# Optimization experiments

Hardware: AMD Instinct MI355X
Metric: run time of the kernel (lower is better)

Reference implementation:

```python
import jax, jax.numpy as jnp
import numpy as np

N_NODES = 50000
N_EDGES = 800000
NFEAT = 128
NHID = 128
NCLASS = 10
NUM_GRAPHS = 512


def setup_inputs() -> dict:
    key = jax.random.key(0)
    ks = jax.random.split(key, 12)
    x = jax.random.normal(ks[0], (N_NODES, NFEAT), dtype=jnp.float32)
    edge_index = jax.random.randint(ks[1], (2, N_EDGES), 0, N_NODES, dtype=jnp.int64)
    batch = jnp.sort(jax.random.randint(ks[2], (N_NODES,), 0, NUM_GRAPHS, dtype=jnp.int64))
    def glorot(k, fan_in, fan_out):
        lim = np.sqrt(6.0 / (fan_in + fan_out))
        return jax.random.uniform(k, (fan_in, fan_out), jnp.float32, -lim, lim)
    return {
        "x": x, "edge_index": edge_index, "batch": batch,
        "W0": glorot(ks[3], NFEAT, NHID), "b0": jnp.zeros((NHID,), jnp.float32),
        "W1": glorot(ks[4], NHID, NHID), "b1": jnp.zeros((NHID,), jnp.float32),
        "W2": glorot(ks[5], NHID, NHID), "b2": jnp.zeros((NHID,), jnp.float32),
        "lin_w": glorot(ks[6], NHID, NCLASS), "lin_b": jnp.zeros((NCLASS,), jnp.float32),
    }


def _gcn_norm(edge_index, n):
    # PyG GCNConv: add self-loops, symmetric normalization D^-1/2 A D^-1/2
    loop = jnp.arange(n, dtype=edge_index.dtype)
    src = jnp.concatenate([edge_index[0], loop])  # [E+N]
    dst = jnp.concatenate([edge_index[1], loop])
    deg = jax.ops.segment_sum(jnp.ones_like(dst, dtype=jnp.float32), dst, num_segments=n)
    dis = jnp.where(deg > 0, jax.lax.rsqrt(jnp.maximum(deg, 1.0)), 0.0)
    norm = dis[src] * dis[dst]  # [E+N]
    return src, dst, norm


def _gcn_conv(x, W, b, src, dst, norm, n):
    h = x @ W                              # [N, nhid]
    msg = h[src] * norm[:, None]           # gather + scale, [E+N, nhid]
    out = jax.ops.segment_sum(msg, dst, num_segments=n)
    return out + b


def reference(x, edge_index, batch, W0, b0, W1, b1, W2, b2, lin_w, lin_b):
    n = x.shape[0]
    src, dst, norm = _gcn_norm(edge_index, n)
    h = x
    for (W, b) in ((W0, b0), (W1, b1), (W2, b2)):
        h = jax.nn.relu(_gcn_conv(h, W, b, src, dst, norm, n))
    # global mean pool over graphs
    sums = jax.ops.segment_sum(h, batch, num_segments=NUM_GRAPHS)
    cnts = jax.ops.segment_sum(jnp.ones((n,), jnp.float32), batch, num_segments=NUM_GRAPHS)
    pooled = sums / jnp.maximum(cnts, 1.0)[:, None]  # [G, nhid]
    logits = pooled @ lin_w + lin_b
    return jax.nn.log_softmax(logits, axis=-1)
```

## Files before the change

### kernel.cpp

```cpp
#include <hip/hip_runtime.h>
#include <hip/hip_fp16.h>


#define FEAT 128
#define NCLASS 10
#define NB_MAX 512

typedef _Float16 h8 __attribute__((ext_vector_type(8)));
typedef float f4 __attribute__((ext_vector_type(4)));

__device__ inline int swz(int row, int cbyte) { return row * 256 + (cbyte ^ ((row & 7) << 4)); }

__device__ inline void gather_pad4(const h8* __restrict__ Hs, const int* __restrict__ csr,
                                   int s, int e, int lig, float* a0, float* a1) {
  int ep = s + ((e - s + 7) & ~7);
  for (int k = s; k < ep; k += 4) {
    int4 c = *(const int4*)&csr[k];
    h8 v0 = Hs[(size_t)c.x * 16 + lig];
    h8 v1 = Hs[(size_t)c.y * 16 + lig];
    h8 v2 = Hs[(size_t)c.z * 16 + lig];
    h8 v3 = Hs[(size_t)c.w * 16 + lig];
#pragma unroll
    for (int j = 0; j < 8; ++j) a0[j] += (float)v0[j];
#pragma unroll
    for (int j = 0; j < 8; ++j) a1[j] += (float)v1[j];
#pragma unroll
    for (int j = 0; j < 8; ++j) a0[j] += (float)v2[j];
#pragma unroll
    for (int j = 0; j < 8; ++j) a1[j] += (float)v3[j];
  }
}

__global__ void __launch_bounds__(256) prep_kernel(const int* __restrict__ ei,
                                                   int* __restrict__ bhist,
                                                   int ne, int nb, int epb, int hb,
                                                   const float* __restrict__ W0,
                                                   const float* __restrict__ W1,
                                                   const float* __restrict__ W2,
                                                   _Float16* __restrict__ Wt, int wtb,
                                                   const int* __restrict__ batch,
                                                   int* __restrict__ gstart, int n, int g) {
  int t = threadIdx.x;
  if (blockIdx.x >= hb + wtb) {
    int i = (blockIdx.x - hb - wtb) * 256 + t;
    if (i >= n) return;
    int bi = batch[i];
    int bp = (i == 0) ? -1 : batch[i - 1];
    for (int q = bp + 1; q <= bi; ++q) gstart[q] = i;
    if (i == n - 1)
      for (int q = bi + 1; q <= g; ++q) gstart[q] = n;
    return;
  }
  if (blockIdx.x >= hb) {
    int i = (blockIdx.x - hb) * 256 + t;
    if (i < 3 * FEAT * FEAT) {
      int l = i / (FEAT * FEAT);
      int r = i - l * (FEAT * FEAT);
      int nn = r >> 7, kk = r & 127;
      const float* W = (l == 0) ? W0 : (l == 1) ? W1 : W2;
      Wt[i] = (_Float16)W[kk * FEAT + nn];
    }
    return;
  }
  __shared__ int lh[NB_MAX];
  for (int i = t; i < nb; i += 256) lh[i] = 0;
  __syncthreads();
  int r0 = blockIdx.x * epb;
  int r1 = min(r0 + epb, ne);
  for (int k = r0 + t; k < r1; k += 256) atomicAdd(&lh[ei[ne + k] >> 7], 1);
  __syncthreads();
  for (int i = t; i < nb; i += 256)
    if (lh[i]) atomicAdd(&bhist[i], lh[i]);
}

__global__ void __launch_bounds__(512) bscan_kernel(const int* __restrict__ bhist,
                                                    int* __restrict__ bstart,
                                                    int* __restrict__ bcur,
                                                    int nb, int ne) {
  __shared__ int sh[512];
  int t = threadIdx.x;
  int v = (t < nb) ? bhist[t] : 0;
  sh[t] = v;
  __syncthreads();
  int x = v;
  for (int d = 1; d < 512; d <<= 1) {
    int y = (t >= d) ? sh[t - d] : 0;
    __syncthreads();
    x += y;
    sh[t] = x;
    __syncthreads();
  }
  if (t < nb) {
    bstart[t] = x - v;
    bcur[t] = x - v;
  }
  if (t == 0) bstart[nb] = ne;
}

__global__ void __launch_bounds__(256) scatter_kernel(const int* __restrict__ ei,
                                                      int* __restrict__ bcur,
                                                      unsigned* __restrict__ buf,
                                                      int ne, int nb, int epb) {
  __shared__ int lh[NB_MAX], lbs[NB_MAX];
  int t = threadIdx.x;
  for (int i = t; i < nb; i += 256) lh[i] = 0;
  __syncthreads();
  int r0 = blockIdx.x * epb;
  int r1 = min(r0 + epb, ne);
  for (int k = r0 + t; k < r1; k += 256) atomicAdd(&lh[ei[ne + k] >> 7], 1);
  __syncthreads();
  for (int i = t; i < nb; i += 256) {
    int c = lh[i];
    lbs[i] = c ? atomicAdd(&bcur[i], c) : 0;
    lh[i] = 0;
  }
  __syncthreads();
  for (int k = r0 + t; k < r1; k += 256) {
    int src = ei[k];
    int dst = ei[ne + k];
    int b = dst >> 7;
    int p = lbs[b] + atomicAdd(&lh[b], 1);
    buf[p] = (unsigned)src | ((unsigned)(dst & 127) << 25);
  }
}

__global__ void __launch_bounds__(256) bucket_build_kernel(const unsigned* __restrict__ buf,
                                                           const int* __restrict__ bstart,
                                                           int2* __restrict__ offend,
                                                           int* __restrict__ csr,
                                                           float* __restrict__ dis, int n) {
  __shared__ int cnt[128], cur[128], sh[128], ps[128];
  int b = blockIdx.x, t = threadIdx.x;
  int e0 = bstart[b], e1 = bstart[b + 1];
  int pb = ((e0 + 7) & ~7) + 1024 * b;
  if (t < 128) cnt[t] = 0;
  __syncthreads();
  for (int k = e0 + t; k < e1; k += 256) atomicAdd(&cnt[buf[k] >> 25], 1);
  __syncthreads();
  int v = 0, pdv = 0;
  if (t < 128) {
    v = cnt[t];
    pdv = (v + 7) & ~7;
    sh[t] = pdv;
  }
  __syncthreads();
  int x = pdv;
  for (int d = 1; d < 128; d <<= 1) {
    int y = (t < 128 && t >= d) ? sh[t - d] : 0;
    __syncthreads();
    if (t < 128) {
      x += y;
      sh[t] = x;
    }
    __syncthreads();
  }
  if (t < 128) {
    int node = (b << 7) + t;
    int st = x - pdv;
    ps[t] = st;
    cur[t] = st;
    if (node < n) {
      offend[node] = make_int2(pb + st, pb + st + v);
      dis[node] = rsqrtf((float)(v + 1));
    }
  }
  __syncthreads();
  for (int k = e0 + t; k < e1; k += 256) {
    unsigned u = buf[k];
    int d = u >> 25;
    int p = atomicAdd(&cur[d], 1);
    csr[pb + p] = (int)(u & 0x1FFFFFFu);
  }
  __syncthreads();
  if (t < 128) {
    int pd = (cnt[t] + 7) & ~7;
    for (int q = cnt[t]; q < pd; ++q) csr[pb + ps[t] + q] = n;
  }
}

__global__ void __launch_bounds__(256) gemm_mfma_kernel(const float* __restrict__ Xf,
                                                        const _Float16* __restrict__ Wt,
                                                        const float* __restrict__ dis,
                                                        _Float16* __restrict__ Hs, int n) {
  __shared__ _Float16 st[64 * FEAT];
  int tid = threadIdx.x;
  int w = tid >> 6, lane = tid & 63;
  int l15 = lane & 15, hi = lane >> 4;

  int rowA = blockIdx.x * 64 + w * 16 + l15;
  int rA = min(rowA, n - 1);

  f4 acc[8];
#pragma unroll
  for (int nb = 0; nb < 8; ++nb) acc[nb] = (f4)(0.f);

#pragma unroll
  for (int kk = 0; kk < FEAT; kk += 32) {
    int ko = kk + hi * 8;
    h8 a;
    float4 x0 = *(const float4*)&Xf[(size_t)rA * FEAT + ko];
    float4 x1 = *(const float4*)&Xf[(size_t)rA * FEAT + ko + 4];
    a[0] = (_Float16)x0.x; a[1] = (_Float16)x0.y; a[2] = (_Float16)x0.z; a[3] = (_Float16)x0.w;
    a[4] = (_Float16)x1.x; a[5] = (_Float16)x1.y; a[6] = (_Float16)x1.z; a[7] = (_Float16)x1.w;
#pragma unroll
    for (int nb = 0; nb < 8; ++nb) {
      h8 bfr = *(const h8*)&Wt[(nb * 16 + l15) * FEAT + ko];
      acc[nb] = __builtin_amdgcn_mfma_f32_16x16x32_f16(a, bfr, acc[nb], 0, 0, 0);
    }
  }

  float dv[4];
#pragma unroll
  for (int r = 0; r < 4; ++r) {
    int grow = blockIdx.x * 64 + w * 16 + hi * 4 + r;
    dv[r] = dis[min(grow, n - 1)];
  }
#pragma unroll
  for (int nb = 0; nb < 8; ++nb)
#pragma unroll
    for (int r = 0; r < 4; ++r)
      st[(w * 16 + hi * 4 + r) * FEAT + nb * 16 + l15] = (_Float16)(acc[nb][r] * dv[r]);
  __syncthreads();

  int rowbase = blockIdx.x * 64;
#pragma unroll
  for (int i = tid; i < 64 * FEAT / 8; i += 256) {
    int row = rowbase + (i >> 4);
    if (row < n)
      *(uint4*)&Hs[(size_t)row * FEAT + (i & 15) * 8] =
          *(const uint4*)&st[(i >> 4) * FEAT + (i & 15) * 8];
  }
}

__global__ void __launch_bounds__(512, 6) fused_kernel(const h8* __restrict__ Hs_in,
                                                       const int* __restrict__ csr,
                                                       const int2* __restrict__ offend,
                                                       const float* __restrict__ dis,
                                                       const float* __restrict__ bias,
                                                       const _Float16* __restrict__ Wt,
                                                       _Float16* __restrict__ Hs_out, int n) {
  __shared__ char xsb[64 * 256];
  int tid = threadIdx.x;
  int w = tid >> 6, lane = tid & 63;
  int grp = lane >> 4, lig = lane & 15;
  int row0 = blockIdx.x * 64;
  int g32 = w * 4 + grp;

  float4 b0 = ((const float4*)bias)[lig * 2];
  float4 b1 = ((const float4*)bias)[lig * 2 + 1];
  float bb[8] = {b0.x, b0.y, b0.z, b0.w, b1.x, b1.y, b1.z, b1.w};

#pragma unroll
  for (int m = 0; m < 2; ++m) {
    int ar = g32 * 2 + m;
    int nd = min(row0 + ar, n - 1);
    int2 oe = offend[nd];
    float a0[8], a1[8];
    h8 v = Hs_in[(size_t)nd * 16 + lig];
#pragma unroll
    for (int j = 0; j < 8; ++j) {
      a0[j] = (float)v[j];
      a1[j] = 0.f;
    }
    gather_pad4(Hs_in, csr, oe.x, oe.y, lig, a0, a1);
    float d = dis[nd];
    h8 o;
#pragma unroll
    for (int j = 0; j < 8; ++j)
      o[j] = (_Float16)fmaxf(fmaf(d, a0[j] + a1[j], bb[j]), 0.f);
    *(h8*)(xsb + swz(ar, lig * 16)) = o;
  }
  __syncthreads();

  int l15 = lane & 15, hi = lane >> 4;
  int strip = w & 3, ch = w >> 2;
  f4 acc[4];
#pragma unroll
  for (int nb = 0; nb < 4; ++nb) acc[nb] = (f4)(0.f);
#pragma unroll
  for (int kk = 0; kk < FEAT; kk += 32) {
    int ko = kk + hi * 8;
    h8 a = *(const h8*)(xsb + swz(strip * 16 + l15, ko * 2));
#pragma unroll
    for (int nb = 0; nb < 4; ++nb) {
      h8 bfr = *(const h8*)&Wt[(ch * 64 + nb * 16 + l15) * FEAT + ko];
      acc[nb] = __builtin_amdgcn_mfma_f32_16x16x32_f16(a, bfr, acc[nb], 0, 0, 0);
    }
  }

  float dv[4];
#pragma unroll
  for (int r = 0; r < 4; ++r) {
    int grow = row0 + strip * 16 + hi * 4 + r;
    dv[r] = dis[min(grow, n - 1)];
  }
  __syncthreads();
#pragma unroll
  for (int nb = 0; nb < 4; ++nb)
#pragma unroll
    for (int r = 0; r < 4; ++r) {
      int srow = strip * 16 + hi * 4 + r;
      *(_Float16*)(xsb + swz(srow, (ch * 64 + nb * 16 + l15) * 2)) =
          (_Float16)(acc[nb][r] * dv[r]);
    }
  __syncthreads();
#pragma unroll
  for (int i = tid; i < 64 * FEAT / 8; i += 512) {
    int row = row0 + (i >> 4);
    if (row < n)
      *(uint4*)&Hs_out[(size_t)row * FEAT + (i & 15) * 8] =
          *(const uint4*)(xsb + swz(i >> 4, (i & 15) * 16));
  }
}

__global__ void __launch_bounds__(512, 6) agg_kernel(const h8* __restrict__ Hs,
                                                     const int* __restrict__ csr,
                                                     const int2* __restrict__ offend,
                                                     const float* __restrict__ dis,
                                                     const float* __restrict__ bias,
                                                     h8* __restrict__ out, int n) {
  int tid = threadIdx.x;
  int g32 = tid >> 4, lig = tid & 15;
  int row0 = blockIdx.x * 64;

  float4 b0 = ((const float4*)bias)[lig * 2];
  float4 b1 = ((const float4*)bias)[lig * 2 + 1];
  float bb[8] = {b0.x, b0.y, b0.z, b0.w, b1.x, b1.y, b1.z, b1.w};

#pragma unroll
  for (int m = 0; m < 2; ++m) {
    int node = row0 + g32 * 2 + m;
    if (node < n) {
      int2 oe = offend[node];
      float a0[8], a1[8];
      h8 v = Hs[(size_t)node * 16 + lig];
#pragma unroll
      for (int j = 0; j < 8; ++j) {
        a0[j] = (float)v[j];
        a1[j] = 0.f;
      }
      gather_pad4(Hs, csr, oe.x, oe.y, lig, a0, a1);
      float d = dis[node];
      h8 o;
#pragma unroll
      for (int j = 0; j < 8; ++j)
        o[j] = (_Float16)fmaxf(fmaf(d, a0[j] + a1[j], bb[j]), 0.f);
      out[(size_t)node * 16 + lig] = o;
    }
  }
}

__global__ void __launch_bounds__(128) pool_kernel(const __half* __restrict__ h,
                                                   const int* __restrict__ gstart,
                                                   const float* __restrict__ lw,
                                                   const float* __restrict__ lb,
                                                   float* __restrict__ out) {
  int g = blockIdx.x;
  int t = threadIdx.x;
  int s = gstart[g];
  int e = gstart[g + 1];
  float a0 = 0.f, a1 = 0.f, a2 = 0.f, a3 = 0.f;
  int i = s;
  for (; i + 4 <= e; i += 4) {
    a0 += __half2float(h[(size_t)i * FEAT + t]);
    a1 += __half2float(h[(size_t)(i + 1) * FEAT + t]);
    a2 += __half2float(h[(size_t)(i + 2) * FEAT + t]);
    a3 += __half2float(h[(size_t)(i + 3) * FEAT + t]);
  }
  for (; i < e; ++i) a0 += __half2float(h[(size_t)i * FEAT + t]);
  float acc = a0 + a1 + a2 + a3;
  float cnt = (float)(e - s);
  float pooled = acc / fmaxf(cnt, 1.f);
  __shared__ float lds[FEAT];
  __shared__ float logits[NCLASS];
  lds[t] = pooled;
  __syncthreads();
  if (t < NCLASS) {
    float z = lb[t];
    for (int k = 0; k < FEAT; ++k) z += lds[k] * lw[k * NCLASS + t];
    logits[t] = z;
  }
  __syncthreads();
  if (t < NCLASS) {
    float m = logits[0];
#pragma unroll
    for (int c = 1; c < NCLASS; ++c) m = fmaxf(m, logits[c]);
    float ssum = 0.f;
#pragma unroll
    for (int c = 0; c < NCLASS; ++c) ssum += expf(logits[c] - m);
    out[(size_t)g * NCLASS + t] = logits[t] - m - logf(ssum);
  }
}

extern "C" void kernel_launch(void* const* d_in, const int* in_sizes, int n_in,
                              void* d_out, int out_size, void* d_ws, size_t ws_size,
                              hipStream_t stream) {
  const float* x = (const float*)d_in[0];
  const int* ei = (const int*)d_in[1];
  const int* batch = (const int*)d_in[2];
  const float* W0 = (const float*)d_in[3];
  const float* b0 = (const float*)d_in[4];
  const float* W1 = (const float*)d_in[5];
  const float* b1 = (const float*)d_in[6];
  const float* W2 = (const float*)d_in[7];
  const float* b2 = (const float*)d_in[8];
  const float* lw = (const float*)d_in[9];
  const float* lb = (const float*)d_in[10];

  int n = in_sizes[2];
  int ne = in_sizes[1] / 2;
  int g = out_size / NCLASS;
  int nb = (n + 127) >> 7;
  int hblocks = 120;
  int epb = (ne + hblocks - 1) / hblocks;
  int wtblocks = (3 * FEAT * FEAT + 255) / 256;
  int bndblocks = (n + 255) / 256;

  char* ws = (char*)d_ws;
  size_t p = 0;
  auto alloc = [&](size_t bytes) {
    size_t cur = p;
    p += (bytes + 255) & ~(size_t)255;
    return cur;
  };
  int2* offend = (int2*)(ws + alloc((size_t)n * 8));
  int* csr = (int*)(ws + alloc(((size_t)ne + 1024 * nb + 64) * 4));
  int* bhist = (int*)(ws + alloc((size_t)NB_MAX * 4));
  int* bstart = (int*)(ws + alloc((size_t)(NB_MAX + 1) * 4));
  int* bcur = (int*)(ws + alloc((size_t)NB_MAX * 4));
  int* gstart = (int*)(ws + alloc((size_t)(g + 1) * 4));
  float* dis = (float*)(ws + alloc((size_t)n * 4));
  unsigned* buf = (unsigned*)(ws + alloc((size_t)ne * 4));
  _Float16* Wt = (_Float16*)(ws + alloc((size_t)3 * FEAT * FEAT * 2));
  _Float16* HA = (_Float16*)(ws + alloc((size_t)(n + 1) * FEAT * 2));
  _Float16* HB = (_Float16*)(ws + alloc((size_t)(n + 1) * FEAT * 2));

  hipMemsetAsync(bhist, 0, NB_MAX * 4, stream);
  hipMemsetAsync(HA + (size_t)n * FEAT, 0, FEAT * 2, stream);
  hipMemsetAsync(HB + (size_t)n * FEAT, 0, FEAT * 2, stream);

  prep_kernel<<<hblocks + wtblocks + bndblocks, 256, 0, stream>>>(
      ei, bhist, ne, nb, epb, hblocks, W0, W1, W2, Wt, wtblocks, batch, gstart, n, g);
  bscan_kernel<<<1, 512, 0, stream>>>(bhist, bstart, bcur, nb, ne);
  scatter_kernel<<<hblocks, 256, 0, stream>>>(ei, bcur, buf, ne, nb, epb);
  bucket_build_kernel<<<nb, 256, 0, stream>>>(buf, bstart, offend, csr, dis, n);

  int gblocks = (n + 63) / 64;
  gemm_mfma_kernel<<<gblocks, 256, 0, stream>>>(x, Wt, dis, HA, n);
  fused_kernel<<<gblocks, 512, 0, stream>>>((const h8*)HA, csr, offend, dis, b0,
                                            Wt + (size_t)1 * FEAT * FEAT, HB, n);
  fused_kernel<<<gblocks, 512, 0, stream>>>((const h8*)HB, csr, offend, dis, b1,
                                            Wt + (size_t)2 * FEAT * FEAT, HA, n);
  agg_kernel<<<gblocks, 512, 0, stream>>>((const h8*)HA, csr, offend, dis, b2, (h8*)HB, n);

  pool_kernel<<<g, 128, 0, stream>>>((const __half*)HB, gstart, lw, lb, (float*)d_out);
}
```

Baseline: 221.9 us.

## Split hidden features into four column-quarter planes for cache-local gathers

Stores the fp16 hidden matrices as four separate planes of 32 features each, so each gather pass touches only a 3.2MB quarter table that fits better in L2. The aggregation loops now iterate over the quarters and load 4 bytes per lane instead of 16. CSR padding drops from multiples of 8 to multiples of 4, and the memset of the padding row moves into the prep kernel. The cost is four passes over the CSR indices and narrower per-lane loads, which issue more memory instructions per edge.

Result: slower. 238.2 us (+7.3%).

```diff
diff --git a/kernel.cpp b/kernel.cpp
--- a/kernel.cpp
+++ b/kernel.cpp
@@ -11,24 +11,9 @@
 
 __device__ inline int swz(int row, int cbyte) { return row * 256 + (cbyte ^ ((row & 7) << 4)); }
 
-__device__ inline void gather_pad4(const h8* __restrict__ Hs, const int* __restrict__ csr,
-                                   int s, int e, int lig, float* a0, float* a1) {
-  int ep = s + ((e - s + 7) & ~7);
-  for (int k = s; k < ep; k += 4) {
-    int4 c = *(const int4*)&csr[k];
-    h8 v0 = Hs[(size_t)c.x * 16 + lig];
-    h8 v1 = Hs[(size_t)c.y * 16 + lig];
-    h8 v2 = Hs[(size_t)c.z * 16 + lig];
-    h8 v3 = Hs[(size_t)c.w * 16 + lig];
-#pragma unroll
-    for (int j = 0; j < 8; ++j) a0[j] += (float)v0[j];
-#pragma unroll
-    for (int j = 0; j < 8; ++j) a1[j] += (float)v1[j];
-#pragma unroll
-    for (int j = 0; j < 8; ++j) a0[j] += (float)v2[j];
-#pragma unroll
-    for (int j = 0; j < 8; ++j) a1[j] += (float)v3[j];
-  }
+__device__ inline float2 uh2f2(unsigned u) {
+  __half2 h = *reinterpret_cast<__half2*>(&u);
+  return make_float2(__low2float(h), __high2float(h));
 }
 
 __global__ void __launch_bounds__(256) prep_kernel(const int* __restrict__ ei,
@@ -39,8 +24,18 @@
                                                    const float* __restrict__ W2,
                                                    _Float16* __restrict__ Wt, int wtb,
                                                    const int* __restrict__ batch,
-                                                   int* __restrict__ gstart, int n, int g) {
+                                                   int* __restrict__ gstart, int n, int g,
+                                                   unsigned* __restrict__ HQA32,
+                                                   unsigned* __restrict__ HQB32, int nblk) {
   int t = threadIdx.x;
+  if (blockIdx.x == nblk - 1) {
+    if (t < 128) {
+      unsigned* H = (t >> 6) ? HQB32 : HQA32;
+      int q = (t >> 4) & 3;
+      H[(size_t)q * (n + 1) * 16 + (size_t)n * 16 + (t & 15)] = 0u;
+    }
+    return;
+  }
   if (blockIdx.x >= hb + wtb) {
     int i = (blockIdx.x - hb - wtb) * 256 + t;
     if (i >= n) return;
@@ -140,7 +135,7 @@
   int v = 0, pdv = 0;
   if (t < 128) {
     v = cnt[t];
-    pdv = (v + 7) & ~7;
+    pdv = (v + 3) & ~3;
     sh[t] = pdv;
   }
   __syncthreads();
@@ -173,7 +168,7 @@
   }
   __syncthreads();
   if (t < 128) {
-    int pd = (cnt[t] + 7) & ~7;
+    int pd = (cnt[t] + 3) & ~3;
     for (int q = cnt[t]; q < pd; ++q) csr[pb + ps[t] + q] = n;
   }
 }
@@ -181,7 +176,7 @@
 __global__ void __launch_bounds__(256) gemm_mfma_kernel(const float* __restrict__ Xf,
                                                         const _Float16* __restrict__ Wt,
                                                         const float* __restrict__ dis,
-                                                        _Float16* __restrict__ Hs, int n) {
+                                                        uint4* __restrict__ H4, int n) {
   __shared__ _Float16 st[64 * FEAT];
   int tid = threadIdx.x;
   int w = tid >> 6, lane = tid & 63;
@@ -223,22 +218,23 @@
   __syncthreads();
 
   int rowbase = blockIdx.x * 64;
-#pragma unroll
-  for (int i = tid; i < 64 * FEAT / 8; i += 256) {
+  int qs4 = (n + 1) * 4;
+#pragma unroll
+  for (int i = tid; i < 64 * 16; i += 256) {
     int row = rowbase + (i >> 4);
+    int c = i & 15, q = c >> 2;
     if (row < n)
-      *(uint4*)&Hs[(size_t)row * FEAT + (i & 15) * 8] =
-          *(const uint4*)&st[(i >> 4) * FEAT + (i & 15) * 8];
-  }
-}
-
-__global__ void __launch_bounds__(512, 6) fused_kernel(const h8* __restrict__ Hs_in,
+      H4[(size_t)q * qs4 + row * 4 + (c & 3)] = *(const uint4*)&st[(i >> 4) * FEAT + c * 8];
+  }
+}
+
+__global__ void __launch_bounds__(512, 6) fused_kernel(const unsigned* __restrict__ HQin,
                                                        const int* __restrict__ csr,
                                                        const int2* __restrict__ offend,
                                                        const float* __restrict__ dis,
                                                        const float* __restrict__ bias,
                                                        const _Float16* __restrict__ Wt,
-                                                       _Float16* __restrict__ Hs_out, int n) {
+                                                       uint4* __restrict__ H4out, int n) {
   __shared__ char xsb[64 * 256];
   int tid = threadIdx.x;
   int w = tid >> 6, lane = tid & 63;
@@ -246,29 +242,45 @@
   int row0 = blockIdx.x * 64;
   int g32 = w * 4 + grp;
 
-  float4 b0 = ((const float4*)bias)[lig * 2];
-  float4 b1 = ((const float4*)bias)[lig * 2 + 1];
-  float bb[8] = {b0.x, b0.y, b0.z, b0.w, b1.x, b1.y, b1.z, b1.w};
-
+  int nds[2];
+  int2 oes[2];
+  float ds[2];
 #pragma unroll
   for (int m = 0; m < 2; ++m) {
-    int ar = g32 * 2 + m;
-    int nd = min(row0 + ar, n - 1);
-    int2 oe = offend[nd];
-    float a0[8], a1[8];
-    h8 v = Hs_in[(size_t)nd * 16 + lig];
-#pragma unroll
-    for (int j = 0; j < 8; ++j) {
-      a0[j] = (float)v[j];
-      a1[j] = 0.f;
-    }
-    gather_pad4(Hs_in, csr, oe.x, oe.y, lig, a0, a1);
-    float d = dis[nd];
-    h8 o;
-#pragma unroll
-    for (int j = 0; j < 8; ++j)
-      o[j] = (_Float16)fmaxf(fmaf(d, a0[j] + a1[j], bb[j]), 0.f);
-    *(h8*)(xsb + swz(ar, lig * 16)) = o;
+    nds[m] = min(row0 + g32 * 2 + m, n - 1);
+    oes[m] = offend[nds[m]];
+    ds[m] = dis[nds[m]];
+  }
+  int qstep = (n + 1) * 16;
+
+  for (int q = 0; q < 4; ++q) {
+    const unsigned* T = HQin + (size_t)q * qstep;
+    float2 bq = ((const float2*)bias)[q * 16 + lig];
+#pragma unroll
+    for (int m = 0; m < 2; ++m) {
+      int nd = nds[m];
+      float2 sv = uh2f2(T[(size_t)nd * 16 + lig]);
+      float ax = sv.x, ay = sv.y, bx = 0.f, by = 0.f;
+      int s = oes[m].x;
+      int ep = s + ((oes[m].y - s + 3) & ~3);
+      for (int k = s; k < ep; k += 4) {
+        int4 c = *(const int4*)&csr[k];
+        unsigned u0 = T[(size_t)c.x * 16 + lig];
+        unsigned u1 = T[(size_t)c.y * 16 + lig];
+        unsigned u2 = T[(size_t)c.z * 16 + lig];
+        unsigned u3 = T[(size_t)c.w * 16 + lig];
+        float2 v0 = uh2f2(u0), v1 = uh2f2(u1), v2 = uh2f2(u2), v3 = uh2f2(u3);
+        ax += v0.x; ay += v0.y;
+        bx += v1.x; by += v1.y;
+        ax += v2.x; ay += v2.y;
+        bx += v3.x; by += v3.y;
+      }
+      float ox = fmaxf(fmaf(ds[m], ax + bx, bq.x), 0.f);
+      float oy = fmaxf(fmaf(ds[m], ay + by, bq.y), 0.f);
+      __half2 hv = __floats2half2_rn(ox, oy);
+      int ar = g32 * 2 + m;
+      *(unsigned*)(xsb + swz(ar, q * 64 + lig * 4)) = *(unsigned*)&hv;
+    }
   }
   __syncthreads();
 
@@ -304,48 +316,67 @@
           (_Float16)(acc[nb][r] * dv[r]);
     }
   __syncthreads();
-#pragma unroll
-  for (int i = tid; i < 64 * FEAT / 8; i += 512) {
+  int qs4 = (n + 1) * 4;
+#pragma unroll
+  for (int i = tid; i < 64 * 16; i += 512) {
     int row = row0 + (i >> 4);
+    int c = i & 15, q = c >> 2;
     if (row < n)
-      *(uint4*)&Hs_out[(size_t)row * FEAT + (i & 15) * 8] =
-          *(const uint4*)(xsb + swz(i >> 4, (i & 15) * 16));
-  }
-}
-
-__global__ void __launch_bounds__(512, 6) agg_kernel(const h8* __restrict__ Hs,
+      H4out[(size_t)q * qs4 + row * 4 + (c & 3)] =
+          *(const uint4*)(xsb + swz(i >> 4, c * 16));
+  }
+}
+
+__global__ void __launch_bounds__(512, 6) agg_kernel(const unsigned* __restrict__ HQin,
                                                      const int* __restrict__ csr,
                                                      const int2* __restrict__ offend,
                                                      const float* __restrict__ dis,
                                                      const float* __restrict__ bias,
-                                                     h8* __restrict__ out, int n) {
+                                                     unsigned* __restrict__ out32, int n) {
   int tid = threadIdx.x;
   int g32 = tid >> 4, lig = tid & 15;
   int row0 = blockIdx.x * 64;
 
-  float4 b0 = ((const float4*)bias)[lig * 2];
-  float4 b1 = ((const float4*)bias)[lig * 2 + 1];
-  float bb[8] = {b0.x, b0.y, b0.z, b0.w, b1.x, b1.y, b1.z, b1.w};
-
+  int nds[2];
+  int2 oes[2];
+  float ds[2];
+  bool val[2];
 #pragma unroll
   for (int m = 0; m < 2; ++m) {
     int node = row0 + g32 * 2 + m;
-    if (node < n) {
-      int2 oe = offend[node];
-      float a0[8], a1[8];
-      h8 v = Hs[(size_t)node * 16 + lig];
-#pragma unroll
-      for (int j = 0; j < 8; ++j) {
-        a0[j] = (float)v[j];
-        a1[j] = 0.f;
+    val[m] = node < n;
+    nds[m] = min(node, n - 1);
+    oes[m] = offend[nds[m]];
+    ds[m] = dis[nds[m]];
+  }
+  int qstep = (n + 1) * 16;
+
+  for (int q = 0; q < 4; ++q) {
+    const unsigned* T = HQin + (size_t)q * qstep;
+    float2 bq = ((const float2*)bias)[q * 16 + lig];
+#pragma unroll
+    for (int m = 0; m < 2; ++m) {
+      int nd = nds[m];
+      float2 sv = uh2f2(T[(size_t)nd * 16 + lig]);
+      float ax = sv.x, ay = sv.y, bx = 0.f, by = 0.f;
+      int s = oes[m].x;
+      int ep = s + ((oes[m].y - s + 3) & ~3);
+      for (int k = s; k < ep; k += 4) {
+        int4 c = *(const int4*)&csr[k];
+        unsigned u0 = T[(size_t)c.x * 16 + lig];
+        unsigned u1 = T[(size_t)c.y * 16 + lig];
+        unsigned u2 = T[(size_t)c.z * 16 + lig];
+        unsigned u3 = T[(size_t)c.w * 16 + lig];
+        float2 v0 = uh2f2(u0), v1 = uh2f2(u1), v2 = uh2f2(u2), v3 = uh2f2(u3);
+        ax += v0.x; ay += v0.y;
+        bx += v1.x; by += v1.y;
+        ax += v2.x; ay += v2.y;
+        bx += v3.x; by += v3.y;
       }
-      gather_pad4(Hs, csr, oe.x, oe.y, lig, a0, a1);
-      float d = dis[node];
-      h8 o;
-#pragma unroll
-      for (int j = 0; j < 8; ++j)
-        o[j] = (_Float16)fmaxf(fmaf(d, a0[j] + a1[j], bb[j]), 0.f);
-      out[(size_t)node * 16 + lig] = o;
+      float ox = fmaxf(fmaf(ds[m], ax + bx, bq.x), 0.f);
+      float oy = fmaxf(fmaf(ds[m], ay + by, bq.y), 0.f);
+      __half2 hv = __floats2half2_rn(ox, oy);
+      if (val[m]) out32[(size_t)nds[m] * 64 + q * 16 + lig] = *(unsigned*)&hv;
     }
   }
 }
@@ -415,6 +446,7 @@
   int epb = (ne + hblocks - 1) / hblocks;
   int wtblocks = (3 * FEAT * FEAT + 255) / 256;
   int bndblocks = (n + 255) / 256;
+  int prep_total = hblocks + wtblocks + bndblocks + 1;
 
   char* ws = (char*)d_ws;
   size_t p = 0;
@@ -432,26 +464,26 @@
   float* dis = (float*)(ws + alloc((size_t)n * 4));
   unsigned* buf = (unsigned*)(ws + alloc((size_t)ne * 4));
   _Float16* Wt = (_Float16*)(ws + alloc((size_t)3 * FEAT * FEAT * 2));
-  _Float16* HA = (_Float16*)(ws + alloc((size_t)(n + 1) * FEAT * 2));
-  _Float16* HB = (_Float16*)(ws + alloc((size_t)(n + 1) * FEAT * 2));
+  unsigned* HQA = (unsigned*)(ws + alloc((size_t)(n + 1) * FEAT * 2));
+  unsigned* HQB = (unsigned*)(ws + alloc((size_t)(n + 1) * FEAT * 2));
+  unsigned* HR = (unsigned*)(ws + alloc((size_t)n * FEAT * 2));
 
   hipMemsetAsync(bhist, 0, NB_MAX * 4, stream);
-  hipMemsetAsync(HA + (size_t)n * FEAT, 0, FEAT * 2, stream);
-  hipMemsetAsync(HB + (size_t)n * FEAT, 0, FEAT * 2, stream);
-
-  prep_kernel<<<hblocks + wtblocks + bndblocks, 256, 0, stream>>>(
-      ei, bhist, ne, nb, epb, hblocks, W0, W1, W2, Wt, wtblocks, batch, gstart, n, g);
+
+  prep_kernel<<<prep_total, 256, 0, stream>>>(ei, bhist, ne, nb, epb, hblocks, W0, W1, W2,
+                                              Wt, wtblocks, batch, gstart, n, g, HQA, HQB,
+                                              prep_total);
   bscan_kernel<<<1, 512, 0, stream>>>(bhist, bstart, bcur, nb, ne);
   scatter_kernel<<<hblocks, 256, 0, stream>>>(ei, bcur, buf, ne, nb, epb);
   bucket_build_kernel<<<nb, 256, 0, stream>>>(buf, bstart, offend, csr, dis, n);
 
   int gblocks = (n + 63) / 64;
-  gemm_mfma_kernel<<<gblocks, 256, 0, stream>>>(x, Wt, dis, HA, n);
-  fused_kernel<<<gblocks, 512, 0, stream>>>((const h8*)HA, csr, offend, dis, b0,
-                                            Wt + (size_t)1 * FEAT * FEAT, HB, n);
-  fused_kernel<<<gblocks, 512, 0, stream>>>((const h8*)HB, csr, offend, dis, b1,
-                                            Wt + (size_t)2 * FEAT * FEAT, HA, n);
-  agg_kernel<<<gblocks, 512, 0, stream>>>((const h8*)HA, csr, offend, dis, b2, (h8*)HB, n);
-
-  pool_kernel<<<g, 128, 0, stream>>>((const __half*)HB, gstart, lw, lb, (float*)d_out);
-}
+  gemm_mfma_kernel<<<gblocks, 256, 0, stream>>>(x, Wt, dis, (uint4*)HQA, n);
+  fused_kernel<<<gblocks, 512, 0, stream>>>(HQA, csr, offend, dis, b0,
+                                            Wt + (size_t)1 * FEAT * FEAT, (uint4*)HQB, n);
+  fused_kernel<<<gblocks, 512, 0, stream>>>(HQB, csr, offend, dis, b1,
+                                            Wt + (size_t)2 * FEAT * FEAT, (uint4*)HQA, n);
+  agg_kernel<<<gblocks, 512, 0, stream>>>(HQA, csr, offend, dis, b2, HR, n);
+
+  pool_kernel<<<g, 128, 0, stream>>>((const __half*)HR, gstart, lw, lb, (float*)d_out);
+}
```

## Partition CSR neighbors by source-range chunks and sync blocks per chunk for L2 locality

Applied to the files above, without the earlier changes.

The CSR build now sorts each node's neighbors into four source-index ranges, each padded to a multiple of four, and stores per-chunk offsets. The gather loops in fused_kernel and agg_kernel walk the chunks in order with a __syncthreads between chunks. Workgroups then move through the feature table roughly in step, so the active working set of the random gathers is about a quarter of the table and should hit L2 or the MALL more often. The cost is more padding, extra metadata loads, block barriers that make each block wait for its slowest wave in every chunk, and a single accumulator chain per node instead of two.

Result: no change. 219.7 us (-1.0%).

```diff
diff --git a/kernel.cpp b/kernel.cpp
--- a/kernel.cpp
+++ b/kernel.cpp
@@ -10,26 +10,6 @@
 typedef float f4 __attribute__((ext_vector_type(4)));
 
 __device__ inline int swz(int row, int cbyte) { return row * 256 + (cbyte ^ ((row & 7) << 4)); }
-
-__device__ inline void gather_pad4(const h8* __restrict__ Hs, const int* __restrict__ csr,
-                                   int s, int e, int lig, float* a0, float* a1) {
-  int ep = s + ((e - s + 7) & ~7);
-  for (int k = s; k < ep; k += 4) {
-    int4 c = *(const int4*)&csr[k];
-    h8 v0 = Hs[(size_t)c.x * 16 + lig];
-    h8 v1 = Hs[(size_t)c.y * 16 + lig];
-    h8 v2 = Hs[(size_t)c.z * 16 + lig];
-    h8 v3 = Hs[(size_t)c.w * 16 + lig];
-#pragma unroll
-    for (int j = 0; j < 8; ++j) a0[j] += (float)v0[j];
-#pragma unroll
-    for (int j = 0; j < 8; ++j) a1[j] += (float)v1[j];
-#pragma unroll
-    for (int j = 0; j < 8; ++j) a0[j] += (float)v2[j];
-#pragma unroll
-    for (int j = 0; j < 8; ++j) a1[j] += (float)v3[j];
-  }
-}
 
 __global__ void __launch_bounds__(256) prep_kernel(const int* __restrict__ ei,
                                                    int* __restrict__ bhist,
@@ -126,25 +106,40 @@
 
 __global__ void __launch_bounds__(256) bucket_build_kernel(const unsigned* __restrict__ buf,
                                                            const int* __restrict__ bstart,
-                                                           int2* __restrict__ offend,
+                                                           int4* __restrict__ off4,
+                                                           int* __restrict__ oend,
                                                            int* __restrict__ csr,
-                                                           float* __restrict__ dis, int n) {
-  __shared__ int cnt[128], cur[128], sh[128], ps[128];
+                                                           float* __restrict__ dis,
+                                                           int n, int csize) {
+  __shared__ int cnt[512], cur[512], loc[512], sh[128];
   int b = blockIdx.x, t = threadIdx.x;
   int e0 = bstart[b], e1 = bstart[b + 1];
-  int pb = ((e0 + 7) & ~7) + 1024 * b;
-  if (t < 128) cnt[t] = 0;
-  __syncthreads();
-  for (int k = e0 + t; k < e1; k += 256) atomicAdd(&cnt[buf[k] >> 25], 1);
-  __syncthreads();
-  int v = 0, pdv = 0;
+  int pb = ((e0 + 7) & ~7) + 2048 * b;
+  for (int i = t; i < 512; i += 256) cnt[i] = 0;
+  __syncthreads();
+  for (int k = e0 + t; k < e1; k += 256) {
+    unsigned u = buf[k];
+    int src = (int)(u & 0x1FFFFFFu);
+    int d = u >> 25;
+    int c = (src >= 3 * csize) ? 3 : (src >= 2 * csize) ? 2 : (src >= csize) ? 1 : 0;
+    atomicAdd(&cnt[d * 4 + c], 1);
+  }
+  __syncthreads();
+  int tot = 0;
   if (t < 128) {
-    v = cnt[t];
-    pdv = (v + 7) & ~7;
-    sh[t] = pdv;
-  }
-  __syncthreads();
-  int x = pdv;
+    int p0 = (cnt[t * 4 + 0] + 3) & ~3;
+    int p1 = (cnt[t * 4 + 1] + 3) & ~3;
+    int p2 = (cnt[t * 4 + 2] + 3) & ~3;
+    int p3 = (cnt[t * 4 + 3] + 3) & ~3;
+    loc[t * 4 + 0] = 0;
+    loc[t * 4 + 1] = p0;
+    loc[t * 4 + 2] = p0 + p1;
+    loc[t * 4 + 3] = p0 + p1 + p2;
+    tot = p0 + p1 + p2 + p3;
+    sh[t] = tot;
+  }
+  __syncthreads();
+  int x = tot;
   for (int d = 1; d < 128; d <<= 1) {
     int y = (t < 128 && t >= d) ? sh[t - d] : 0;
     __syncthreads();
@@ -155,26 +150,39 @@
     __syncthreads();
   }
   if (t < 128) {
+    int st = pb + x - tot;
     int node = (b << 7) + t;
-    int st = x - pdv;
-    ps[t] = st;
-    cur[t] = st;
+    int s0 = st + loc[t * 4 + 0], s1 = st + loc[t * 4 + 1];
+    int s2 = st + loc[t * 4 + 2], s3 = st + loc[t * 4 + 3];
+    cur[t * 4 + 0] = s0;
+    cur[t * 4 + 1] = s1;
+    cur[t * 4 + 2] = s2;
+    cur[t * 4 + 3] = s3;
     if (node < n) {
-      offend[node] = make_int2(pb + st, pb + st + v);
+      off4[node] = make_int4(s0, s1, s2, s3);
+      oend[node] = st + tot;
+      int v = cnt[t * 4] + cnt[t * 4 + 1] + cnt[t * 4 + 2] + cnt[t * 4 + 3];
       dis[node] = rsqrtf((float)(v + 1));
     }
   }
   __syncthreads();
   for (int k = e0 + t; k < e1; k += 256) {
     unsigned u = buf[k];
+    int src = (int)(u & 0x1FFFFFFu);
     int d = u >> 25;
-    int p = atomicAdd(&cur[d], 1);
-    csr[pb + p] = (int)(u & 0x1FFFFFFu);
+    int c = (src >= 3 * csize) ? 3 : (src >= 2 * csize) ? 2 : (src >= csize) ? 1 : 0;
+    int p = atomicAdd(&cur[d * 4 + c], 1);
+    csr[p] = src;
   }
   __syncthreads();
   if (t < 128) {
-    int pd = (cnt[t] + 7) & ~7;
-    for (int q = cnt[t]; q < pd; ++q) csr[pb + ps[t] + q] = n;
+#pragma unroll
+    for (int c = 0; c < 4; ++c) {
+      int k0 = t * 4 + c;
+      int pad = ((cnt[k0] + 3) & ~3) - cnt[k0];
+      int base = cur[k0];
+      for (int q = 0; q < pad; ++q) csr[base + q] = n;
+    }
   }
 }
 
@@ -234,7 +242,8 @@
 
 __global__ void __launch_bounds__(512, 6) fused_kernel(const h8* __restrict__ Hs_in,
                                                        const int* __restrict__ csr,
-                                                       const int2* __restrict__ offend,
+                                                       const int4* __restrict__ off4,
+                                                       const int* __restrict__ oend,
                                                        const float* __restrict__ dis,
                                                        const float* __restrict__ bias,
                                                        const _Float16* __restrict__ Wt,
@@ -246,30 +255,61 @@
   int row0 = blockIdx.x * 64;
   int g32 = w * 4 + grp;
 
-  float4 b0 = ((const float4*)bias)[lig * 2];
-  float4 b1 = ((const float4*)bias)[lig * 2 + 1];
-  float bb[8] = {b0.x, b0.y, b0.z, b0.w, b1.x, b1.y, b1.z, b1.w};
-
-#pragma unroll
-  for (int m = 0; m < 2; ++m) {
-    int ar = g32 * 2 + m;
-    int nd = min(row0 + ar, n - 1);
-    int2 oe = offend[nd];
-    float a0[8], a1[8];
-    h8 v = Hs_in[(size_t)nd * 16 + lig];
-#pragma unroll
-    for (int j = 0; j < 8; ++j) {
-      a0[j] = (float)v[j];
-      a1[j] = 0.f;
-    }
-    gather_pad4(Hs_in, csr, oe.x, oe.y, lig, a0, a1);
-    float d = dis[nd];
-    h8 o;
-#pragma unroll
-    for (int j = 0; j < 8; ++j)
-      o[j] = (_Float16)fmaxf(fmaf(d, a0[j] + a1[j], bb[j]), 0.f);
-    *(h8*)(xsb + swz(ar, lig * 16)) = o;
-  }
+  int nd0 = min(row0 + g32 * 2, n - 1);
+  int nd1 = min(row0 + g32 * 2 + 1, n - 1);
+  int4 o0 = off4[nd0], o1 = off4[nd1];
+  int oe0 = oend[nd0], oe1 = oend[nd1];
+
+  float acc0[8], acc1[8];
+  h8 sv0 = Hs_in[(size_t)nd0 * 16 + lig];
+  h8 sv1 = Hs_in[(size_t)nd1 * 16 + lig];
+#pragma unroll
+  for (int j = 0; j < 8; ++j) {
+    acc0[j] = (float)sv0[j];
+    acc1[j] = (float)sv1[j];
+  }
+
+#pragma unroll
+  for (int c = 0; c < 4; ++c) {
+    int s0 = (c == 0) ? o0.x : (c == 1) ? o0.y : (c == 2) ? o0.z : o0.w;
+    int e0 = (c == 0) ? o0.y : (c == 1) ? o0.z : (c == 2) ? o0.w : oe0;
+    for (int k = s0; k < e0; k += 4) {
+      int4 ci = *(const int4*)&csr[k];
+      h8 v0 = Hs_in[(size_t)ci.x * 16 + lig];
+      h8 v1 = Hs_in[(size_t)ci.y * 16 + lig];
+      h8 v2 = Hs_in[(size_t)ci.z * 16 + lig];
+      h8 v3 = Hs_in[(size_t)ci.w * 16 + lig];
+#pragma unroll
+      for (int j = 0; j < 8; ++j)
+        acc0[j] += ((float)v0[j] + (float)v1[j]) + ((float)v2[j] + (float)v3[j]);
+    }
+    int s1 = (c == 0) ? o1.x : (c == 1) ? o1.y : (c == 2) ? o1.z : o1.w;
+    int e1 = (c == 0) ? o1.y : (c == 1) ? o1.z : (c == 2) ? o1.w : oe1;
+    for (int k = s1; k < e1; k += 4) {
+      int4 ci = *(const int4*)&csr[k];
+      h8 v0 = Hs_in[(size_t)ci.x * 16 + lig];
+      h8 v1 = Hs_in[(size_t)ci.y * 16 + lig];
+      h8 v2 = Hs_in[(size_t)ci.z * 16 + lig];
+      h8 v3 = Hs_in[(size_t)ci.w * 16 + lig];
+#pragma unroll
+      for (int j = 0; j < 8; ++j)
+        acc1[j] += ((float)v0[j] + (float)v1[j]) + ((float)v2[j] + (float)v3[j]);
+    }
+    __syncthreads();
+  }
+
+  float d0 = dis[nd0], d1 = dis[nd1];
+  float4 bb0 = ((const float4*)bias)[lig * 2];
+  float4 bb1 = ((const float4*)bias)[lig * 2 + 1];
+  float bb[8] = {bb0.x, bb0.y, bb0.z, bb0.w, bb1.x, bb1.y, bb1.z, bb1.w};
+  h8 oA, oB;
+#pragma unroll
+  for (int j = 0; j < 8; ++j) {
+    oA[j] = (_Float16)fmaxf(fmaf(d0, acc0[j], bb[j]), 0.f);
+    oB[j] = (_Float16)fmaxf(fmaf(d1, acc1[j], bb[j]), 0.f);
+  }
+  *(h8*)(xsb + swz(g32 * 2, lig * 16)) = oA;
+  *(h8*)(xsb + swz(g32 * 2 + 1, lig * 16)) = oB;
   __syncthreads();
 
   int l15 = lane & 15, hi = lane >> 4;
@@ -315,7 +355,8 @@
 
 __global__ void __launch_bounds__(512, 6) agg_kernel(const h8* __restrict__ Hs,
                                                      const int* __restrict__ csr,
-                                                     const int2* __restrict__ offend,
+                                                     const int4* __restrict__ off4,
+                                                     const int* __restrict__ oend,
                                                      const float* __restrict__ dis,
                                                      const float* __restrict__ bias,
                                                      h8* __restrict__ out, int n) {
@@ -323,31 +364,61 @@
   int g32 = tid >> 4, lig = tid & 15;
   int row0 = blockIdx.x * 64;
 
-  float4 b0 = ((const float4*)bias)[lig * 2];
-  float4 b1 = ((const float4*)bias)[lig * 2 + 1];
-  float bb[8] = {b0.x, b0.y, b0.z, b0.w, b1.x, b1.y, b1.z, b1.w};
-
-#pragma unroll
-  for (int m = 0; m < 2; ++m) {
-    int node = row0 + g32 * 2 + m;
-    if (node < n) {
-      int2 oe = offend[node];
-      float a0[8], a1[8];
-      h8 v = Hs[(size_t)node * 16 + lig];
-#pragma unroll
-      for (int j = 0; j < 8; ++j) {
-        a0[j] = (float)v[j];
-        a1[j] = 0.f;
-      }
-      gather_pad4(Hs, csr, oe.x, oe.y, lig, a0, a1);
-      float d = dis[node];
-      h8 o;
+  int node0 = row0 + g32 * 2, node1 = node0 + 1;
+  int nd0 = min(node0, n - 1), nd1 = min(node1, n - 1);
+  int4 o0 = off4[nd0], o1 = off4[nd1];
+  int oe0 = oend[nd0], oe1 = oend[nd1];
+
+  float acc0[8], acc1[8];
+  h8 sv0 = Hs[(size_t)nd0 * 16 + lig];
+  h8 sv1 = Hs[(size_t)nd1 * 16 + lig];
+#pragma unroll
+  for (int j = 0; j < 8; ++j) {
+    acc0[j] = (float)sv0[j];
+    acc1[j] = (float)sv1[j];
+  }
+
+#pragma unroll
+  for (int c = 0; c < 4; ++c) {
+    int s0 = (c == 0) ? o0.x : (c == 1) ? o0.y : (c == 2) ? o0.z : o0.w;
+    int e0 = (c == 0) ? o0.y : (c == 1) ? o0.z : (c == 2) ? o0.w : oe0;
+    for (int k = s0; k < e0; k += 4) {
+      int4 ci = *(const int4*)&csr[k];
+      h8 v0 = Hs[(size_t)ci.x * 16 + lig];
+      h8 v1 = Hs[(size_t)ci.y * 16 + lig];
+      h8 v2 = Hs[(size_t)ci.z * 16 + lig];
+      h8 v3 = Hs[(size_t)ci.w * 16 + lig];
 #pragma unroll
       for (int j = 0; j < 8; ++j)
-        o[j] = (_Float16)fmaxf(fmaf(d, a0[j] + a1[j], bb[j]), 0.f);
-      out[(size_t)node * 16 + lig] = o;
-    }
-  }
+        acc0[j] += ((float)v0[j] + (float)v1[j]) + ((float)v2[j] + (float)v3[j]);
+    }
+    int s1 = (c == 0) ? o1.x : (c == 1) ? o1.y : (c == 2) ? o1.z : o1.w;
+    int e1 = (c == 0) ? o1.y : (c == 1) ? o1.z : (c == 2) ? o1.w : oe1;
+    for (int k = s1; k < e1; k += 4) {
+      int4 ci = *(const int4*)&csr[k];
+      h8 v0 = Hs[(size_t)ci.x * 16 + lig];
+      h8 v1 = Hs[(size_t)ci.y * 16 + lig];
+      h8 v2 = Hs[(size_t)ci.z * 16 + lig];
+      h8 v3 = Hs[(size_t)ci.w * 16 + lig];
+#pragma unroll
+      for (int j = 0; j < 8; ++j)
+        acc1[j] += ((float)v0[j] + (float)v1[j]) + ((float)v2[j] + (float)v3[j]);
+    }
+    __syncthreads();
+  }
+
+  float d0 = dis[nd0], d1 = dis[nd1];
+  float4 bb0 = ((const float4*)bias)[lig * 2];
+  float4 bb1 = ((const float4*)bias)[lig * 2 + 1];
+  float bb[8] = {bb0.x, bb0.y, bb0.z, bb0.w, bb1.x, bb1.y, bb1.z, bb1.w};
+  h8 oA, oB;
+#pragma unroll
+  for (int j = 0; j < 8; ++j) {
+    oA[j] = (_Float16)fmaxf(fmaf(d0, acc0[j], bb[j]), 0.f);
+    oB[j] = (_Float16)fmaxf(fmaf(d1, acc1[j], bb[j]), 0.f);
+  }
+  if (node0 < n) out[(size_t)node0 * 16 + lig] = oA;
+  if (node1 < n) out[(size_t)node1 * 16 + lig] = oB;
 }
 
 __global__ void __launch_bounds__(128) pool_kernel(const __half* __restrict__ h,
@@ -411,6 +482,7 @@
   int ne = in_sizes[1] / 2;
   int g = out_size / NCLASS;
   int nb = (n + 127) >> 7;
+  int csize = (n + 3) / 4;
   int hblocks = 120;
   int epb = (ne + hblocks - 1) / hblocks;
   int wtblocks = (3 * FEAT * FEAT + 255) / 256;
@@ -423,8 +495,9 @@
     p += (bytes + 255) & ~(size_t)255;
     return cur;
   };
-  int2* offend = (int2*)(ws + alloc((size_t)n * 8));
-  int* csr = (int*)(ws + alloc(((size_t)ne + 1024 * nb + 64) * 4));
+  int4* off4 = (int4*)(ws + alloc((size_t)n * 16));
+  int* oend = (int*)(ws + alloc((size_t)n * 4));
+  int* csr = (int*)(ws + alloc(((size_t)ne + 2048 * (size_t)nb + 64) * 4));
   int* bhist = (int*)(ws + alloc((size_t)NB_MAX * 4));
   int* bstart = (int*)(ws + alloc((size_t)(NB_MAX + 1) * 4));
   int* bcur = (int*)(ws + alloc((size_t)NB_MAX * 4));
@@ -443,15 +516,16 @@
       ei, bhist, ne, nb, epb, hblocks, W0, W1, W2, Wt, wtblocks, batch, gstart, n, g);
   bscan_kernel<<<1, 512, 0, stream>>>(bhist, bstart, bcur, nb, ne);
   scatter_kernel<<<hblocks, 256, 0, stream>>>(ei, bcur, buf, ne, nb, epb);
-  bucket_build_kernel<<<nb, 256, 0, stream>>>(buf, bstart, offend, csr, dis, n);
+  bucket_build_kernel<<<nb, 256, 0, stream>>>(buf, bstart, off4, oend, csr, dis, n, csize);
 
   int gblocks = (n + 63) / 64;
   gemm_mfma_kernel<<<gblocks, 256, 0, stream>>>(x, Wt, dis, HA, n);
-  fused_kernel<<<gblocks, 512, 0, stream>>>((const h8*)HA, csr, offend, dis, b0,
+  fused_kernel<<<gblocks, 512, 0, stream>>>((const h8*)HA, csr, off4, oend, dis, b0,
                                             Wt + (size_t)1 * FEAT * FEAT, HB, n);
-  fused_kernel<<<gblocks, 512, 0, stream>>>((const h8*)HB, csr, offend, dis, b1,
+  fused_kernel<<<gblocks, 512, 0, stream>>>((const h8*)HB, csr, off4, oend, dis, b1,
                                             Wt + (size_t)2 * FEAT * FEAT, HA, n);
-  agg_kernel<<<gblocks, 512, 0, stream>>>((const h8*)HA, csr, offend, dis, b2, (h8*)HB, n);
+  agg_kernel<<<gblocks, 512, 0, stream>>>((const h8*)HA, csr, off4, oend, dis, b2,
+                                          (h8*)HB, n);
 
   pool_kernel<<<g, 128, 0, stream>>>((const __half*)HB, gstart, lw, lb, (float*)d_out);
 }
```
